# Kernel optimization log

Measured on AMD Instinct MI355X. Metric: run time of the kernel, lower is better.

Reference implementation:

```python
import jax, jax.numpy as jnp
import numpy as np

# ---- model hyperparameters (match init_kwargs) ----
NUM_INPUT, NUM_HIDDEN, NUM_OUTPUT = 2048, 65536, 512
FAN_OUT = 256
TAU, THRESHOLD = 20.0, 0.3
SPIKE_DELAY = 1  # must be 1 for the one-step-delay scan formulation below
N = NUM_INPUT + NUM_HIDDEN + NUM_OUTPUT
HID_START, OUT_START = NUM_INPUT, NUM_INPUT + NUM_HIDDEN
SURROGATE_SCALE = 25.0


@jax.custom_vjp
def spike(v):
    """Heaviside spike with sigmoid surrogate gradient (SurrogateSpike)."""
    return (v >= THRESHOLD).astype(v.dtype)

def _spike_fwd(v):
    return spike(v), v

def _spike_bwd(v, g):
    s = jax.nn.sigmoid(SURROGATE_SCALE * (v - THRESHOLD))
    return (g * SURROGATE_SCALE * s * (1.0 - s),)

spike.defvjp(_spike_fwd, _spike_bwd)


def make_targets(seed=42):
    """Structured random connectivity (mirrors _generate_random_targets ranges)."""
    rng = np.random.default_rng(seed)
    t = np.empty((N, FAN_OUT), dtype=np.int64)
    # input neurons -> hidden
    t[:NUM_INPUT] = rng.integers(HID_START, OUT_START, size=(NUM_INPUT, FAN_OUT))
    # hidden neurons -> hidden+output, excluding self
    hid = rng.integers(HID_START, N, size=(NUM_HIDDEN, FAN_OUT))
    src = np.arange(HID_START, OUT_START)[:, None]
    R = N - HID_START
    hid = np.where(hid == src, HID_START + (hid - HID_START + 1) % R, hid)
    t[HID_START:OUT_START] = hid
    # output neurons -> hidden
    t[OUT_START:] = rng.integers(HID_START, OUT_START, size=(NUM_OUTPUT, FAN_OUT))
    return jnp.asarray(t, dtype=jnp.int32)


def setup_inputs() -> dict:
    key = jax.random.key(0)
    k1, k2 = jax.random.split(key)
    weights = jax.random.normal(k1, (N, FAN_OUT), dtype=jnp.float32) * 0.3
    input_spikes = jax.random.bernoulli(k2, 0.2, (NUM_INPUT,))
    return {"input_spikes": input_spikes, "weights": weights,
            "targets": make_targets(), "max_timesteps": 50}


def _simulate(input_spikes, weights, targets, max_timesteps):
    decay_base = jnp.exp(jnp.float32(-1.0 / TAU))
    idx = jnp.arange(N)
    flat_targets = targets.reshape(-1)  # [N*FAN_OUT]

    inp = jnp.zeros(N, bool).at[:NUM_INPUT].set(input_spikes)
    pot = jnp.zeros(N, jnp.float32)
    last_update = jnp.zeros(N, jnp.int32)
    has_fired = inp
    strength = jnp.where(inp, 2.0, 0.0).astype(jnp.float32)
    out_times = jnp.full(NUM_OUTPUT, -1, jnp.int32)
    fire_now = inp  # input spikes scheduled on the wheel at t=0

    def step(carry, t):
        pot, last_update, has_fired, strength, fire_now, out_times = carry
        # contributions of spiking sources: spike_strength[src] * weights[src]
        src_val = jnp.where(fire_now, strength, 0.0)                 # [N]
        contrib = (src_val[:, None] * weights).reshape(-1)           # [N*FAN_OUT]
        # neurons that receive at least one spike this step (the 'unique_targets')
        hits = jnp.zeros(N, jnp.float32).at[flat_targets].add(
            jnp.repeat(fire_now.astype(jnp.float32), FAN_OUT))
        is_target = hits > 0
        # lazy retroactive decay only on touched neurons
        dt = (t - last_update).astype(jnp.float32)
        pot = jnp.where(is_target, pot * decay_base ** dt, pot)
        last_update = jnp.where(is_target, t, last_update)
        # scatter-add contributions (zeros for non-firing sources)
        pot = pot.at[flat_targets].add(contrib)
        # spike check with refractory mask
        probs = spike(pot) * (1.0 - has_fired.astype(jnp.float32))
        new_fired = probs > 0.5
        has_fired = has_fired | new_fired
        strength = jnp.where(new_fired, probs, strength)
        out_times = jnp.where(new_fired[OUT_START:] & (out_times < 0), t, out_times)
        # schedule hidden spikes for delivery at t + 1 (spike_delay == 1)
        fire_next = new_fired & (idx < OUT_START)
        # reset membrane of newly fired non-output neurons
        reset = jnp.where(idx >= OUT_START, 0.0, probs)
        pot = pot * (1.0 - reset)
        return (pot, last_update, has_fired, strength, fire_next, out_times), None

    carry = (pot, last_update, has_fired, strength, fire_now, out_times)
    carry, _ = jax.lax.scan(step, carry, jnp.arange(max_timesteps, dtype=jnp.int32))
    pot, last_update, has_fired, strength, _, out_times = carry
    # final decay to end of simulation window
    final_dt = (max_timesteps - last_update).astype(jnp.float32)
    pot = pot * decay_base ** final_dt
    return out_times, pot[OUT_START:]


def reference(input_spikes, weights, targets, max_timesteps):
    out_times, out_pot = _simulate(input_spikes, weights, targets, max_timesteps)
    return out_times, out_pot
```

## Files before the change

kernel.cpp:

```cpp
#include <hip/hip_runtime.h>
#include <math.h>

#define N_TOTAL    68096
#define NUM_INPUT  2048
#define NUM_OUTPUT 512
#define OUT_START  67584
#define N_TGT      66048
#define NUM_HIDDEN 65536
#define FB_WORDS   2048
#define FAN_OUT    256
#define THRESH     0.3f
#define T_MAX      50
#define T_BIG      12
#define BM_WORDS   2064
#define LIST_CAP   12288

#define HALF_SZ    33024
#define N_CHUNK    128
#define DENSE_THR  6000


__device__ __forceinline__ int calc_chunks(int fcnt) {
    int c = fcnt >> 7;
    if (c < 1) c = 1;
    if (c > N_CHUNK) c = N_CHUNK;
    return c;
}

__global__ __launch_bounds__(256) void init_k(
    const unsigned int* __restrict__ in0,
    float* pot, float* acc, int* last_up, unsigned char* fired,
    int* frontier0, int* cnt, float* out_f, float* decay_tab,
    unsigned* fbits)
{
    __shared__ int sF, sG;
    const int tid = threadIdx.x;
    if (tid == 0) { sF = 0; sG = 0; }
    __syncthreads();
    for (int k = tid; k < 512; k += 256) {
        unsigned int v = in0[k];
        if (v == 0x3F800000u) atomicAdd(&sF, 1);
        else if (v > 1u)      sG = 1;
    }
    __syncthreads();
    const int mode = (sF >= 8) ? 1 : (sG ? 2 : 0);

    const int i = blockIdx.x * 256 + tid;
    const int lane = tid & 63;
    if (i <= T_MAX) {
        float base = expf(-0.05f);
        decay_tab[i] = (float)pow((double)base, (double)i);
    }
    if (i < NUM_OUTPUT) out_f[i] = -1.0f;
    if (i < FB_WORDS)   fbits[i] = 0u;
    bool want = false;
    if (i < N_TOTAL) {
        pot[i] = 0.0f;
        acc[i] = 0.0f;
        last_up[i] = 0;
        bool s = false;
        if (i < NUM_INPUT) {
            if (mode == 0)      s = ((const int*)in0)[i] != 0;
            else if (mode == 1) s = ((const float*)in0)[i] != 0.0f;
            else                s = ((const unsigned char*)in0)[i] != 0;
        }
        fired[i] = s ? 1 : 0;
        want = s;
    }
    unsigned long long m = __ballot(want);
    if (m) {
        int leader = __ffsll((long long)m) - 1;
        int base = 0;
        if (lane == leader) base = atomicAdd(&cnt[0], __popcll(m));
        base = __shfl(base, leader, 64);
        if (want) {
            int off = __popcll(m & ((1ull << (unsigned)lane) - 1ull));
            frontier0[base + off] = i;
        }
    }
}

#define LIVE(SFB, TG) ({ int b_ = (TG) - NUM_INPUT; \
    (b_ >= NUM_HIDDEN) || !((SFB[b_ >> 5] >> (b_ & 31)) & 1u); })

__global__ __launch_bounds__(1024) void step_scatter_k(
    const int* __restrict__ fr, const int* __restrict__ cnt_cur,
    int* cnt_next,
    const int* __restrict__ targets, const float* __restrict__ weights,
    float* __restrict__ acc, float* __restrict__ rep,
    const unsigned* __restrict__ fbits)
{
    __shared__ float    lacc[HALF_SZ];
    __shared__ unsigned sfb[FB_WORDS];
    const int fcnt = *cnt_cur;
    const int tid  = threadIdx.x;
    if (blockIdx.x == 0 && tid == 0) *cnt_next = 0;
    if (fcnt == 0) return;

    for (int k = tid; k < FB_WORDS; k += 1024) sfb[k] = fbits[k];

    if (fcnt < DENSE_THR) {
        __syncthreads();
        const int nq = fcnt * (FAN_OUT / 4);
        const int stride = gridDim.x * 1024;
        for (int q = blockIdx.x * 1024 + tid; q < nq; q += stride) {
            int s  = fr[q >> 6];
            int j4 = (q & 63) << 2;
            const int base = s * FAN_OUT + j4;
            int4 tg = *(const int4*)(targets + base);
            const bool lx = LIVE(sfb, tg.x), ly = LIVE(sfb, tg.y);
            const bool lz = LIVE(sfb, tg.z), lw = LIVE(sfb, tg.w);
            if (lx | ly | lz | lw) {
                float4 wv = *(const float4*)(weights + base);
                float  st = (s < NUM_INPUT) ? 2.0f : 1.0f;
                if (lx) atomicAdd(&acc[tg.x], st * wv.x);
                if (ly) atomicAdd(&acc[tg.y], st * wv.y);
                if (lz) atomicAdd(&acc[tg.z], st * wv.z);
                if (lw) atomicAdd(&acc[tg.w], st * wv.w);
            }
        }
        return;
    }

    const int chunks = calc_chunks(fcnt);
    const int c = blockIdx.x & 127;
    const int h = blockIdx.x >> 7;
    if (c >= chunks) return;
    const int base = NUM_INPUT + h * HALF_SZ;
    for (int k = tid; k < HALF_SZ / 4; k += 1024)
        ((float4*)lacc)[k] = make_float4(0.f, 0.f, 0.f, 0.f);
    __syncthreads();
    const int lo = (int)(((long long)fcnt * c)       / chunks);
    const int hi = (int)(((long long)fcnt * (c + 1)) / chunks);
    const int nq = (hi - lo) << 6;
    for (int q = tid; q < nq; q += 2048) {
        const int q2 = q + 1024;
        const bool hasB = q2 < nq;
        const int sA  = fr[lo + (q >> 6)];
        const int sB  = hasB ? fr[lo + (q2 >> 6)] : sA;
        const int ebA = sA * FAN_OUT + ((q  & 63) << 2);
        const int ebB = sB * FAN_OUT + ((q2 & 63) << 2);
        int4 tgA = *(const int4*)(targets + ebA);
        int4 tgB = *(const int4*)(targets + ebB);
        int x;
        {
            x = tgA.x - base; const bool kx = (unsigned)x < HALF_SZ && LIVE(sfb, tgA.x);
            int y = tgA.y - base; const bool ky = (unsigned)y < HALF_SZ && LIVE(sfb, tgA.y);
            int z = tgA.z - base; const bool kz = (unsigned)z < HALF_SZ && LIVE(sfb, tgA.z);
            int u = tgA.w - base; const bool ku = (unsigned)u < HALF_SZ && LIVE(sfb, tgA.w);
            if (kx | ky | kz | ku) {
                float4 wv = *(const float4*)(weights + ebA);
                const float st = (sA < NUM_INPUT) ? 2.0f : 1.0f;
                if (kx) atomicAdd(&lacc[x], st * wv.x);
                if (ky) atomicAdd(&lacc[y], st * wv.y);
                if (kz) atomicAdd(&lacc[z], st * wv.z);
                if (ku) atomicAdd(&lacc[u], st * wv.w);
            }
        }
        if (hasB) {
            x = tgB.x - base; const bool kx = (unsigned)x < HALF_SZ && LIVE(sfb, tgB.x);
            int y = tgB.y - base; const bool ky = (unsigned)y < HALF_SZ && LIVE(sfb, tgB.y);
            int z = tgB.z - base; const bool kz = (unsigned)z < HALF_SZ && LIVE(sfb, tgB.z);
            int u = tgB.w - base; const bool ku = (unsigned)u < HALF_SZ && LIVE(sfb, tgB.w);
            if (kx | ky | kz | ku) {
                float4 wv = *(const float4*)(weights + ebB);
                const float st = (sB < NUM_INPUT) ? 2.0f : 1.0f;
                if (kx) atomicAdd(&lacc[x], st * wv.x);
                if (ky) atomicAdd(&lacc[y], st * wv.y);
                if (kz) atomicAdd(&lacc[z], st * wv.z);
                if (ku) atomicAdd(&lacc[u], st * wv.w);
            }
        }
    }
    __syncthreads();
    float4* out = (float4*)(rep + (size_t)((c << 1) + h) * HALF_SZ);
    for (int k = tid; k < HALF_SZ / 4; k += 1024) out[k] = ((float4*)lacc)[k];
}

__global__ __launch_bounds__(128) void step_update_k(
    const float* __restrict__ rep, const int* __restrict__ cnt_cur,
    float* __restrict__ pot, float* __restrict__ acc,
    int* __restrict__ last_up, unsigned char* __restrict__ fired,
    int* __restrict__ frontier_next, int* __restrict__ cnt_next,
    float* __restrict__ out_f, const float* __restrict__ decay_tab, int t,
    unsigned* __restrict__ fbits)
{
    const int fcnt = *cnt_cur;
    if (fcnt == 0) return;
    const int g = blockIdx.x * 128 + threadIdx.x;
    const int lane = threadIdx.x & 63;
    bool w2 = false;
    const int n = NUM_INPUT + g;
    if (n >= OUT_START || !fired[n]) {
        float a;
        if (fcnt < DENSE_THR) {
            a = acc[n];
            if (a != 0.0f) acc[n] = 0.0f;
        } else {
            const int chunks = calc_chunks(fcnt);
            const int hh  = (g >= HALF_SZ) ? 1 : 0;
            const int idx = g - hh * HALF_SZ;
            const float* p0 = rep + (size_t)hh * HALF_SZ + idx;
            float a0 = 0.f, a1 = 0.f, a2 = 0.f, a3 = 0.f;
            int c = 0;
            for (; c + 3 < chunks; c += 4) {
                a0 += p0[(size_t)((c + 0) << 1) * HALF_SZ];
                a1 += p0[(size_t)((c + 1) << 1) * HALF_SZ];
                a2 += p0[(size_t)((c + 2) << 1) * HALF_SZ];
                a3 += p0[(size_t)((c + 3) << 1) * HALF_SZ];
            }
            for (; c < chunks; ++c)
                a0 += p0[(size_t)(c << 1) * HALF_SZ];
            a = (a0 + a1) + (a2 + a3);
        }
        if (a != 0.0f) {
            float p = pot[n] * decay_tab[t - last_up[n]] + a;
            last_up[n] = t;
            if (!fired[n] && p >= THRESH) {
                fired[n] = 1;
                if (n < OUT_START) {
                    p = 0.0f; w2 = true;
                    const int b = n - NUM_INPUT;
                    atomicOr(&fbits[b >> 5], 1u << (b & 31));
                } else out_f[n - OUT_START] = (float)t;
            }
            pot[n] = p;
        }
    }
    unsigned long long m = __ballot(w2);
    if (m) {
        int leader = __ffsll((long long)m) - 1;
        int base = 0;
        if (lane == leader) base = atomicAdd(cnt_next, __popcll(m));
        base = __shfl(base, leader, 64);
        if (w2) {
            int off = __popcll(m & ((1ull << (unsigned)lane) - 1ull));
            frontier_next[base + off] = n;
        }
    }
}

__global__ __launch_bounds__(1024) void tail_k(
    float* __restrict__ pot, float* __restrict__ acc,
    int* __restrict__ last_up, unsigned char* __restrict__ fired,
    int* __restrict__ fr0, int* __restrict__ fr1, int* __restrict__ cnt,
    const int* __restrict__ targets, const float* __restrict__ weights,
    float* __restrict__ out_f, const float* __restrict__ decay_tab,
    const unsigned* __restrict__ fbits)
{
    __shared__ unsigned bm[BM_WORDS];
    __shared__ unsigned sfb[FB_WORDS];
    __shared__ int      lst[LIST_CAP];
    __shared__ int      lcnt, ovf;
    __shared__ float    sdecay[T_MAX + 1];
    const int tid = threadIdx.x;
    if (tid <= T_MAX) sdecay[tid] = decay_tab[tid];
    for (int k = tid; k < FB_WORDS; k += 1024) sfb[k] = fbits[k];

    for (int t = T_BIG; t < T_MAX; ++t) {
        const int cur = t & 1, nxt = cur ^ 1;
        for (int k = tid; k < BM_WORDS; k += 1024) bm[k] = 0u;
        if (tid == 0) { lcnt = 0; ovf = 0; cnt[nxt] = 0; }
        __syncthreads();
        const int fcnt = cnt[cur];
        if (fcnt == 0) break;
        const int* fr  = (cur == 0) ? fr0 : fr1;
        int*       frn = (cur == 0) ? fr1 : fr0;

        const int nq = fcnt * (FAN_OUT / 4);
        for (int q = tid; q < nq; q += 1024) {
            int s  = fr[q >> 6];
            int j4 = (q & 63) << 2;
            const int base = s * FAN_OUT + j4;
            int4 tg = *(const int4*)(targets + base);
            const bool lx = LIVE(sfb, tg.x), ly = LIVE(sfb, tg.y);
            const bool lz = LIVE(sfb, tg.z), lw = LIVE(sfb, tg.w);
            if (!(lx | ly | lz | lw)) continue;
            float4 wv = *(const float4*)(weights + base);
            float  st = (s < NUM_INPUT) ? 2.0f : 1.0f;
            #define EDGE(L, TG, WV) if (L) {                                  \
                atomicAdd(&acc[TG], st * (WV));                               \
                int b = (TG) - NUM_INPUT;                                     \
                unsigned bit = 1u << (b & 31);                                \
                unsigned old = atomicOr(&bm[b >> 5], bit);                    \
                if (!(old & bit)) {                                           \
                    int p_ = atomicAdd(&lcnt, 1);                             \
                    if (p_ < LIST_CAP) lst[p_] = (TG); else ovf = 1;          \
                } }
            EDGE(lx, tg.x, wv.x); EDGE(ly, tg.y, wv.y);
            EDGE(lz, tg.z, wv.z); EDGE(lw, tg.w, wv.w);
            #undef EDGE
        }
        __syncthreads();

        const int M = lcnt;
        const bool full = (ovf != 0);
        const int lo = full ? (NUM_INPUT + tid) : tid;
        const int hi = full ? N_TOTAL : M;
        for (int k = lo; k < hi; k += 1024) {
            const int n = full ? k : lst[k];
            if (n < OUT_START && fired[n]) continue;
            float a = __hip_atomic_load(&acc[n], __ATOMIC_RELAXED,
                                        __HIP_MEMORY_SCOPE_AGENT);
            if (a != 0.0f) {
                __hip_atomic_store(&acc[n], 0.0f, __ATOMIC_RELAXED,
                                   __HIP_MEMORY_SCOPE_AGENT);
                float p = pot[n] * sdecay[t - last_up[n]] + a;
                last_up[n] = t;
                if (!fired[n] && p >= THRESH) {
                    fired[n] = 1;
                    if (n < OUT_START) {
                        p = 0.0f;
                        int pos = atomicAdd(&cnt[nxt], 1);
                        frn[pos] = n;
                        const int b = n - NUM_INPUT;
                        atomicOr(&sfb[b >> 5], 1u << (b & 31));
                    } else out_f[n - OUT_START] = (float)t;
                }
                pot[n] = p;
            }
        }
        __syncthreads();
    }

    __syncthreads();
    for (int i = tid; i < NUM_OUTPUT; i += 1024) {
        int n = OUT_START + i;
        out_f[NUM_OUTPUT + i] = pot[n] * sdecay[T_MAX - last_up[n]];
    }
}

extern "C" void kernel_launch(void* const* d_in, const int* in_sizes, int n_in,
                              void* d_out, int out_size, void* d_ws, size_t ws_size,
                              hipStream_t stream) {
    const void*  in_spikes = d_in[0];
    const float* weights   = (const float*)d_in[1];
    const int*   targets   = (const int*)d_in[2];
    float*       out_f     = (float*)d_out;

    char* w = (char*)d_ws;
    int*      cnt       = (int*)w;
    float*    decay_tab = (float*)(w + 256);
    float*    pot       = (float*)(w + 512);
    float*    acc       = pot + N_TOTAL;
    int*      last_up   = (int*)(acc + N_TOTAL);
    int*      fr0       = last_up + N_TOTAL;
    int*      fr1       = fr0 + N_TOTAL;
    unsigned* fbits     = (unsigned*)(fr1 + N_TOTAL);
    unsigned char* fired = (unsigned char*)(fbits + FB_WORDS);
    size_t base_bytes = (size_t)((char*)(fired + N_TOTAL) - w);
    size_t rep_off    = (base_bytes + 255) & ~(size_t)255;
    float* rep        = (float*)(w + rep_off);

    hipMemsetAsync(cnt, 0, 16, stream);
    init_k<<<266, 256, 0, stream>>>((const unsigned int*)in_spikes,
                                    pot, acc, last_up, fired,
                                    fr0, cnt, out_f, decay_tab, fbits);

    int* fr[2] = {fr0, fr1};
    for (int t = 0; t < T_BIG; ++t) {
        const int cur = t & 1, nxt = cur ^ 1;
        step_scatter_k<<<2 * N_CHUNK, 1024, 0, stream>>>(
            fr[cur], &cnt[cur], &cnt[nxt], targets, weights, acc, rep, fbits);
        step_update_k<<<516, 128, 0, stream>>>(
            rep, &cnt[cur], pot, acc, last_up, fired,
            fr[nxt], &cnt[nxt], out_f, decay_tab, t, fbits);
    }
    tail_k<<<1, 1024, 0, stream>>>(pot, acc, last_up, fired, fr0, fr1, cnt,
                                   targets, weights, out_f, decay_tab, fbits);
}
```

Measured before the change: 269.4 us.

## Split dense scatter target range into quarters and early-exit idle sparse blocks

In the dense scatter path, each block now privatises a quarter of the target range in LDS instead of half, and the grid is doubled to cover four quarters per chunk. The smaller LDS footprint is meant to allow more blocks per CU, at the cost of each block re-reading its chunk's targets twice as often. The reduce kernel is updated to index the quarter-strided replica layout. In the sparse path, blocks with no work now return before loading the fired bitmap, and each thread handles one item instead of grid-striding, which relies on the enlarged grid covering every item.

```diff
diff --git a/kernel.cpp b/kernel.cpp
--- a/kernel.cpp
+++ b/kernel.cpp
@@ -15,7 +15,7 @@
 #define BM_WORDS   2064
 #define LIST_CAP   12288
 
-#define HALF_SZ    33024
+#define QTR_SZ     16512
 #define N_CHUNK    128
 #define DENSE_THR  6000
 
@@ -90,20 +90,20 @@
     float* __restrict__ acc, float* __restrict__ rep,
     const unsigned* __restrict__ fbits)
 {
-    __shared__ float    lacc[HALF_SZ];
+    __shared__ float    lacc[QTR_SZ];
     __shared__ unsigned sfb[FB_WORDS];
     const int fcnt = *cnt_cur;
     const int tid  = threadIdx.x;
     if (blockIdx.x == 0 && tid == 0) *cnt_next = 0;
     if (fcnt == 0) return;
 
-    for (int k = tid; k < FB_WORDS; k += 1024) sfb[k] = fbits[k];
-
     if (fcnt < DENSE_THR) {
+        const int nq = fcnt * (FAN_OUT / 4);
+        const int q  = blockIdx.x * 1024 + tid;
+        if (blockIdx.x * 1024 >= nq) return;
+        for (int k = tid; k < FB_WORDS; k += 1024) sfb[k] = fbits[k];
         __syncthreads();
-        const int nq = fcnt * (FAN_OUT / 4);
-        const int stride = gridDim.x * 1024;
-        for (int q = blockIdx.x * 1024 + tid; q < nq; q += stride) {
+        if (q < nq) {
             int s  = fr[q >> 6];
             int j4 = (q & 63) << 2;
             const int base = s * FAN_OUT + j4;
@@ -123,11 +123,12 @@
     }
 
     const int chunks = calc_chunks(fcnt);
-    const int c = blockIdx.x & 127;
-    const int h = blockIdx.x >> 7;
+    const int c   = blockIdx.x & 127;
+    const int qtr = blockIdx.x >> 7;
     if (c >= chunks) return;
-    const int base = NUM_INPUT + h * HALF_SZ;
-    for (int k = tid; k < HALF_SZ / 4; k += 1024)
+    for (int k = tid; k < FB_WORDS; k += 1024) sfb[k] = fbits[k];
+    const int base = NUM_INPUT + qtr * QTR_SZ;
+    for (int k = tid; k < QTR_SZ / 4; k += 1024)
         ((float4*)lacc)[k] = make_float4(0.f, 0.f, 0.f, 0.f);
     __syncthreads();
     const int lo = (int)(((long long)fcnt * c)       / chunks);
@@ -142,12 +143,11 @@
         const int ebB = sB * FAN_OUT + ((q2 & 63) << 2);
         int4 tgA = *(const int4*)(targets + ebA);
         int4 tgB = *(const int4*)(targets + ebB);
-        int x;
         {
-            x = tgA.x - base; const bool kx = (unsigned)x < HALF_SZ && LIVE(sfb, tgA.x);
-            int y = tgA.y - base; const bool ky = (unsigned)y < HALF_SZ && LIVE(sfb, tgA.y);
-            int z = tgA.z - base; const bool kz = (unsigned)z < HALF_SZ && LIVE(sfb, tgA.z);
-            int u = tgA.w - base; const bool ku = (unsigned)u < HALF_SZ && LIVE(sfb, tgA.w);
+            int x = tgA.x - base; const bool kx = (unsigned)x < QTR_SZ && LIVE(sfb, tgA.x);
+            int y = tgA.y - base; const bool ky = (unsigned)y < QTR_SZ && LIVE(sfb, tgA.y);
+            int z = tgA.z - base; const bool kz = (unsigned)z < QTR_SZ && LIVE(sfb, tgA.z);
+            int u = tgA.w - base; const bool ku = (unsigned)u < QTR_SZ && LIVE(sfb, tgA.w);
             if (kx | ky | kz | ku) {
                 float4 wv = *(const float4*)(weights + ebA);
                 const float st = (sA < NUM_INPUT) ? 2.0f : 1.0f;
@@ -158,10 +158,10 @@
             }
         }
         if (hasB) {
-            x = tgB.x - base; const bool kx = (unsigned)x < HALF_SZ && LIVE(sfb, tgB.x);
-            int y = tgB.y - base; const bool ky = (unsigned)y < HALF_SZ && LIVE(sfb, tgB.y);
-            int z = tgB.z - base; const bool kz = (unsigned)z < HALF_SZ && LIVE(sfb, tgB.z);
-            int u = tgB.w - base; const bool ku = (unsigned)u < HALF_SZ && LIVE(sfb, tgB.w);
+            int x = tgB.x - base; const bool kx = (unsigned)x < QTR_SZ && LIVE(sfb, tgB.x);
+            int y = tgB.y - base; const bool ky = (unsigned)y < QTR_SZ && LIVE(sfb, tgB.y);
+            int z = tgB.z - base; const bool kz = (unsigned)z < QTR_SZ && LIVE(sfb, tgB.z);
+            int u = tgB.w - base; const bool ku = (unsigned)u < QTR_SZ && LIVE(sfb, tgB.w);
             if (kx | ky | kz | ku) {
                 float4 wv = *(const float4*)(weights + ebB);
                 const float st = (sB < NUM_INPUT) ? 2.0f : 1.0f;
@@ -173,8 +173,8 @@
         }
     }
     __syncthreads();
-    float4* out = (float4*)(rep + (size_t)((c << 1) + h) * HALF_SZ);
-    for (int k = tid; k < HALF_SZ / 4; k += 1024) out[k] = ((float4*)lacc)[k];
+    float4* out = (float4*)(rep + (size_t)((c << 2) + qtr) * QTR_SZ);
+    for (int k = tid; k < QTR_SZ / 4; k += 1024) out[k] = ((float4*)lacc)[k];
 }
 
 __global__ __launch_bounds__(128) void step_update_k(
@@ -198,19 +198,19 @@
             if (a != 0.0f) acc[n] = 0.0f;
         } else {
             const int chunks = calc_chunks(fcnt);
-            const int hh  = (g >= HALF_SZ) ? 1 : 0;
-            const int idx = g - hh * HALF_SZ;
-            const float* p0 = rep + (size_t)hh * HALF_SZ + idx;
+            const int qtr = g / QTR_SZ;
+            const int idx = g - qtr * QTR_SZ;
+            const float* p0 = rep + (size_t)qtr * QTR_SZ + idx;
             float a0 = 0.f, a1 = 0.f, a2 = 0.f, a3 = 0.f;
             int c = 0;
             for (; c + 3 < chunks; c += 4) {
-                a0 += p0[(size_t)((c + 0) << 1) * HALF_SZ];
-                a1 += p0[(size_t)((c + 1) << 1) * HALF_SZ];
-                a2 += p0[(size_t)((c + 2) << 1) * HALF_SZ];
-                a3 += p0[(size_t)((c + 3) << 1) * HALF_SZ];
+                a0 += p0[(size_t)(c + 0) * (4 * QTR_SZ)];
+                a1 += p0[(size_t)(c + 1) * (4 * QTR_SZ)];
+                a2 += p0[(size_t)(c + 2) * (4 * QTR_SZ)];
+                a3 += p0[(size_t)(c + 3) * (4 * QTR_SZ)];
             }
             for (; c < chunks; ++c)
-                a0 += p0[(size_t)(c << 1) * HALF_SZ];
+                a0 += p0[(size_t)c * (4 * QTR_SZ)];
             a = (a0 + a1) + (a2 + a3);
         }
         if (a != 0.0f) {
@@ -360,7 +360,7 @@
     int* fr[2] = {fr0, fr1};
     for (int t = 0; t < T_BIG; ++t) {
         const int cur = t & 1, nxt = cur ^ 1;
-        step_scatter_k<<<2 * N_CHUNK, 1024, 0, stream>>>(
+        step_scatter_k<<<4 * N_CHUNK, 1024, 0, stream>>>(
             fr[cur], &cnt[cur], &cnt[nxt], targets, weights, acc, rep, fbits);
         step_update_k<<<516, 128, 0, stream>>>(
             rep, &cnt[cur], pot, acc, last_up, fired,
```

Measured after the change: 264.9 us. No clear change (-1.7%).
